# Kernel tuning notes

Measured on AMD Instinct MI355X. Metric: run time of the kernel, lower is better.

Reference implementation:

```python
import jax, jax.numpy as jnp
import numpy as np

B, C, NX, NY = 4, 64, 512, 512
N_PER_B = 30000  # non-empty pillars per sample


def setup_inputs() -> dict:
    key = jax.random.key(0)
    voxel_features = jax.random.normal(key, (B * N_PER_B, C), dtype=jnp.float32)
    # Build coords [N,4] = (batch, z, y, x) with unique (x,y) per batch so the
    # scatter-set is deterministic (PointPillars pillar coords are unique).
    rng = np.random.default_rng(0)
    parts = []
    for b in range(B):
        flat = rng.choice(NX * NY, size=N_PER_B, replace=False)
        x = flat // NY
        y = flat % NY
        parts.append(np.stack([np.full(N_PER_B, b, np.int64),
                               np.zeros(N_PER_B, np.int64),
                               y.astype(np.int64),
                               x.astype(np.int64)], axis=1))
    coords = jnp.asarray(np.concatenate(parts, axis=0))
    return {"voxel_features": voxel_features, "coords": coords, "batch_size": B}


def reference(voxel_features, coords, batch_size):
    # Fused single scatter: global flat index = b*nx*ny + x*ny + y
    flat = coords[:, 0] * (NX * NY) + coords[:, 3] * NY + coords[:, 2]  # [N]
    canvas = jnp.zeros((batch_size * NX * NY, C), dtype=voxel_features.dtype)
    canvas = canvas.at[flat].set(voxel_features)  # [B*nx*ny, C]
    # -> [B, C, nx, ny]; reshape (nx, ny) matches index = x*ny + y
    return canvas.reshape(batch_size, NX, NY, C).transpose(0, 3, 1, 2)
```

## Files before the change

kernel.cpp:

```cpp
#include <hip/hip_runtime.h>

#define NXC 512
#define NYC 512
#define CC  64
#define BC  4
#define PLANE (NXC * NYC)

typedef float v4f __attribute__((ext_vector_type(4)));

__global__ void pp_zero_map(int4* __restrict__ map4, int n4) {
    int i = blockIdx.x * blockDim.x + threadIdx.x;
    if (i < n4) map4[i] = make_int4(0, 0, 0, 0);
}

__global__ void pp_build_map(const int* __restrict__ coords, int* __restrict__ map, int N) {
    int n = blockIdx.x * blockDim.x + threadIdx.x;
    if (n >= N) return;
    int4 c = *(const int4*)(coords + 4 * (size_t)n);
    map[((size_t)c.x * NXC + c.w) * NYC + c.z] = n + 1;
}

__global__ void __launch_bounds__(256) pp_gather(const float* __restrict__ vf,
                                                 const int* __restrict__ map,
                                                 const float* __restrict__ zrow,
                                                 float* __restrict__ out) {
    int bx = blockIdx.x;
    int t  = threadIdx.x;
    int b  = bx >> 9;
    int x  = bx & (NXC - 1);

    int c0 = (t >> 7) << 5;
    int y4 = (t & 127) << 2;

    int4 nn = *(const int4*)(map + (size_t)bx * NYC + y4);

    const float* p0 = nn.x ? vf + (size_t)(nn.x - 1) * CC : zrow;
    const float* p1 = nn.y ? vf + (size_t)(nn.y - 1) * CC : zrow;
    const float* p2 = nn.z ? vf + (size_t)(nn.z - 1) * CC : zrow;
    const float* p3 = nn.w ? vf + (size_t)(nn.w - 1) * CC : zrow;

    float* ob = out + ((size_t)(b * CC + c0) * NXC + x) * NYC + y4;

    #pragma unroll
    for (int cg = 0; cg < 8; ++cg) {
        int c = c0 + cg * 4;
        v4f va = *(const v4f*)(p0 + c);
        v4f vb = *(const v4f*)(p1 + c);
        v4f vc = *(const v4f*)(p2 + c);
        v4f vd = *(const v4f*)(p3 + c);
        float* o = ob + (size_t)cg * 4 * PLANE;
        v4f s0 = {va.x, vb.x, vc.x, vd.x};
        v4f s1 = {va.y, vb.y, vc.y, vd.y};
        v4f s2 = {va.z, vb.z, vc.z, vd.z};
        v4f s3 = {va.w, vb.w, vc.w, vd.w};
        __builtin_nontemporal_store(s0, (v4f*)(o));
        __builtin_nontemporal_store(s1, (v4f*)(o + PLANE));
        __builtin_nontemporal_store(s2, (v4f*)(o + 2 * (size_t)PLANE));
        __builtin_nontemporal_store(s3, (v4f*)(o + 3 * (size_t)PLANE));
    }
}

extern "C" void kernel_launch(void* const* d_in, const int* in_sizes, int n_in,
                              void* d_out, int out_size, void* d_ws, size_t ws_size,
                              hipStream_t stream) {
    const float* vf     = (const float*)d_in[0];
    const int*   coords = (const int*)d_in[1];

    float* out  = (float*)d_out;
    int*   map  = (int*)d_ws;
    const int MAPN = BC * NXC * NYC;
    float* zrow = (float*)(map + MAPN);

    const int N = in_sizes[0] / CC;
    const int MAPN4 = MAPN / 4 + 16;

    pp_zero_map<<<(MAPN4 + 255) / 256, 256, 0, stream>>>((int4*)map, MAPN4);
    pp_build_map<<<(N + 255) / 256, 256, 0, stream>>>(coords, map, N);
    pp_gather<<<BC * NXC, 256, 0, stream>>>(vf, map, zrow, out);
}
```

Baseline: 295.1 us.

## Stage occupied pillar features in LDS per row before transposed scatter writes

Each block now compacts the non-empty pillars of its x-row into a shared-memory list, loads their 64-channel features cooperatively with coalesced vector loads into a padded LDS buffer, and then does the transposed output writes by reading from LDS, with a zero row standing in for empty cells. This replaces scattered per-thread global gathers, including repeated reads of the zero row, with one coalesced load per occupied pillar. Rows with more than 128 pillars fall back to direct global loads. It adds three barriers, shared atomics and LDS traffic per block.

```diff
diff --git a/kernel.cpp b/kernel.cpp
--- a/kernel.cpp
+++ b/kernel.cpp
@@ -5,6 +5,8 @@
 #define CC  64
 #define BC  4
 #define PLANE (NXC * NYC)
+#define MAXS 128
+#define PADW 68
 
 typedef float v4f __attribute__((ext_vector_type(4)));
 
@@ -22,32 +24,65 @@
 
 __global__ void __launch_bounds__(256) pp_gather(const float* __restrict__ vf,
                                                  const int* __restrict__ map,
-                                                 const float* __restrict__ zrow,
                                                  float* __restrict__ out) {
+    __shared__ float buf[(MAXS + 1) * PADW];
+    __shared__ int   sy[NYC];
+    __shared__ int   pil[MAXS];
+    __shared__ int   cnt;
+
     int bx = blockIdx.x;
     int t  = threadIdx.x;
+
+    if (t == 0) cnt = 0;
+    if (t < 17) *(v4f*)(&buf[MAXS * PADW + t * 4]) = (v4f){0.f, 0.f, 0.f, 0.f};
+    __syncthreads();
+
+    const int* mrow = map + (size_t)bx * NYC;
+    int2 mv = *(const int2*)(mrow + 2 * t);
+    {
+        int vv[2] = {mv.x, mv.y};
+        #pragma unroll
+        for (int i = 0; i < 2; ++i) {
+            int v = vv[i], e;
+            if (v) {
+                int s = atomicAdd(&cnt, 1);
+                if (s < MAXS) { pil[s] = v - 1; e = s; }
+                else          { e = 0x40000000 | (v - 1); }
+            } else e = MAXS;
+            sy[2 * t + i] = e;
+        }
+    }
+    __syncthreads();
+
+    int K = cnt; if (K > MAXS) K = MAXS;
+    int lane16 = t & 15;
+    for (int s = t >> 4; s < K; s += 16) {
+        v4f f = *(const v4f*)(vf + (size_t)pil[s] * CC + lane16 * 4);
+        *(v4f*)(&buf[s * PADW + lane16 * 4]) = f;
+    }
+    __syncthreads();
+
     int b  = bx >> 9;
     int x  = bx & (NXC - 1);
-
     int c0 = (t >> 7) << 5;
     int y4 = (t & 127) << 2;
 
-    int4 nn = *(const int4*)(map + (size_t)bx * NYC + y4);
-
-    const float* p0 = nn.x ? vf + (size_t)(nn.x - 1) * CC : zrow;
-    const float* p1 = nn.y ? vf + (size_t)(nn.y - 1) * CC : zrow;
-    const float* p2 = nn.z ? vf + (size_t)(nn.z - 1) * CC : zrow;
-    const float* p3 = nn.w ? vf + (size_t)(nn.w - 1) * CC : zrow;
+    int4 e = *(const int4*)(sy + y4);
 
     float* ob = out + ((size_t)(b * CC + c0) * NXC + x) * NYC + y4;
 
     #pragma unroll
     for (int cg = 0; cg < 8; ++cg) {
         int c = c0 + cg * 4;
-        v4f va = *(const v4f*)(p0 + c);
-        v4f vb = *(const v4f*)(p1 + c);
-        v4f vc = *(const v4f*)(p2 + c);
-        v4f vd = *(const v4f*)(p3 + c);
+        v4f va, vb, vc, vd;
+        va = (e.x & 0x40000000) ? *(const v4f*)(vf + (size_t)(e.x & 0x3FFFFFFF) * CC + c)
+                                : *(const v4f*)(&buf[e.x * PADW + c]);
+        vb = (e.y & 0x40000000) ? *(const v4f*)(vf + (size_t)(e.y & 0x3FFFFFFF) * CC + c)
+                                : *(const v4f*)(&buf[e.y * PADW + c]);
+        vc = (e.z & 0x40000000) ? *(const v4f*)(vf + (size_t)(e.z & 0x3FFFFFFF) * CC + c)
+                                : *(const v4f*)(&buf[e.z * PADW + c]);
+        vd = (e.w & 0x40000000) ? *(const v4f*)(vf + (size_t)(e.w & 0x3FFFFFFF) * CC + c)
+                                : *(const v4f*)(&buf[e.w * PADW + c]);
         float* o = ob + (size_t)cg * 4 * PLANE;
         v4f s0 = {va.x, vb.x, vc.x, vd.x};
         v4f s1 = {va.y, vb.y, vc.y, vd.y};
@@ -66,15 +101,14 @@
     const float* vf     = (const float*)d_in[0];
     const int*   coords = (const int*)d_in[1];
 
-    float* out  = (float*)d_out;
-    int*   map  = (int*)d_ws;
-    const int MAPN = BC * NXC * NYC;
-    float* zrow = (float*)(map + MAPN);
+    float* out = (float*)d_out;
+    int*   map = (int*)d_ws;
 
     const int N = in_sizes[0] / CC;
-    const int MAPN4 = MAPN / 4 + 16;
+    const int MAPN  = BC * NXC * NYC;
+    const int MAPN4 = MAPN / 4;
 
     pp_zero_map<<<(MAPN4 + 255) / 256, 256, 0, stream>>>((int4*)map, MAPN4);
     pp_build_map<<<(N + 255) / 256, 256, 0, stream>>>(coords, map, N);
-    pp_gather<<<BC * NXC, 256, 0, stream>>>(vf, map, zrow, out);
+    pp_gather<<<BC * NXC, 256, 0, stream>>>(vf, map, out);
 }
```

Result: no change. 296.5 us (+0.5%).
